# Performance work log

Measured on AMD Instinct MI355X. Metric: run time of the kernel, lower is better.

Reference implementation:

```python
import jax, jax.numpy as jnp
import numpy as np

N_NODES = 262144
N_EDGES = 2097152
N_GRAPHS = 8192
IN_CH = 54
HID = 32
OUT_CH = 64
SLOPE = 0.01  # AttentiveFP uses leaky_relu / GATConv negative_slope=0.01
NUM_TIMESTEPS = 2


def _gru(x, h, wih, whh, bih, bhh):
    # torch.nn.GRUCell semantics
    gi = x @ wih.T + bih
    gh = h @ whh.T + bhh
    ir, iz, inn = jnp.split(gi, 3, axis=-1)
    hr, hz, hn = jnp.split(gh, 3, axis=-1)
    r = jax.nn.sigmoid(ir + hr)
    z = jax.nn.sigmoid(iz + hz)
    n = jnp.tanh(inn + r * hn)
    return (1.0 - z) * n + z * h


def _seg_softmax(a, idx, n):
    # PyG softmax over edges grouped by target index
    m = jax.ops.segment_max(a, idx, num_segments=n)
    e = jnp.exp(a - m[idx])
    s = jax.ops.segment_sum(e, idx, num_segments=n)
    return e / (s[idx] + 1e-16)


def _forward(x, edge_attr,
             lin1_w, lin1_b,
             g_lin1_w, g_lin2_w, g_att_l, g_att_r, g_bias,
             gru1_wih, gru1_whh, gru1_bih, gru1_bhh,
             a_lin_w, a_att_src, a_att_dst, a_bias,
             gru2_wih, gru2_whh, gru2_bih, gru2_bhh,
             m_lin_w, m_att_src, m_att_dst, m_bias,
             gru3_wih, gru3_whh, gru3_bih, gru3_bhh,
             lin2_w, lin2_b,
             edge_index, batch_index):
    src, dst = edge_index[0], edge_index[1]  # j -> i (source_to_target)
    n = x.shape[0]
    # Atom embedding
    x = jax.nn.leaky_relu(x @ lin1_w.T + lin1_b, SLOPE)
    # --- GATEConv (first layer, uses edge features) ---
    xj, xi = x[src], x[dst]
    e = jax.nn.leaky_relu(jnp.concatenate([xj, edge_attr], axis=-1) @ g_lin1_w.T, SLOPE)
    alpha = jax.nn.leaky_relu(e @ g_att_l + xi @ g_att_r, SLOPE)
    alpha = _seg_softmax(alpha, dst, n)
    h = jax.ops.segment_sum((xj @ g_lin2_w.T) * alpha[:, None], dst, num_segments=n) + g_bias
    h = jax.nn.elu(h)
    x = jax.nn.relu(_gru(h, x, gru1_wih, gru1_whh, gru1_bih, gru1_bhh))
    # --- GATConv atom layer (num_layers=2 -> one extra conv) ---
    xt = x @ a_lin_w.T
    al = xt @ a_att_src
    ar = xt @ a_att_dst
    alpha = jax.nn.leaky_relu(al[src] + ar[dst], SLOPE)
    alpha = _seg_softmax(alpha, dst, n)
    h = jax.ops.segment_sum(xt[src] * alpha[:, None], dst, num_segments=n) + a_bias
    h = jax.nn.elu(h)
    x = jax.nn.relu(_gru(h, x, gru2_wih, gru2_whh, gru2_bih, gru2_bhh))
    # --- Molecule readout: iterative GAT attention from nodes to their graph ---
    out = jax.nn.relu(jax.ops.segment_sum(x, batch_index, num_segments=N_GRAPHS))
    xs = x @ m_lin_w.T          # transformed node (source) features, fixed per step
    a_node = xs @ m_att_src     # per-node attention logit contribution
    for _ in range(NUM_TIMESTEPS):
        a_g = (out @ m_lin_w.T) @ m_att_dst  # per-graph contribution
        alpha = jax.nn.leaky_relu(a_node + a_g[batch_index], SLOPE)
        alpha = _seg_softmax(alpha, batch_index, N_GRAPHS)
        h = jax.ops.segment_sum(xs * alpha[:, None], batch_index, num_segments=N_GRAPHS) + m_bias
        h = jax.nn.elu(h)
        out = jax.nn.relu(_gru(h, out, gru3_wih, gru3_whh, gru3_bih, gru3_bhh))
    out = out @ lin2_w.T + lin2_b
    # Mish activation wrapper
    return out * jnp.tanh(jax.nn.softplus(out))


def setup_inputs() -> dict:
    key = jax.random.key(0)
    ks = jax.random.split(key, 24)
    def rn(k, shape, s=0.1):
        return jax.random.normal(k, shape, dtype=jnp.float32) * s
    z = lambda *s: jnp.zeros(s, jnp.float32)
    return {
        "x": jax.random.normal(ks[0], (N_NODES, IN_CH), dtype=jnp.float32),
        "edge_attr": jax.random.normal(ks[1], (N_EDGES, 1), dtype=jnp.float32),
        "edge_index": jax.random.randint(ks[2], (2, N_EDGES), 0, N_NODES, dtype=jnp.int32),
        "batch_index": jnp.sort(jax.random.randint(ks[3], (N_NODES,), 0, N_GRAPHS, dtype=jnp.int32)),
        "lin1_w": rn(ks[4], (HID, IN_CH)), "lin1_b": z(HID),
        "g_lin1_w": rn(ks[5], (HID, HID + 1)),
        "g_lin2_w": rn(ks[6], (HID, HID)),
        "g_att_l": rn(ks[7], (HID,)), "g_att_r": rn(ks[8], (HID,)),
        "g_bias": z(HID),
        "gru1_wih": rn(ks[9], (3 * HID, HID)), "gru1_whh": rn(ks[10], (3 * HID, HID)),
        "gru1_bih": z(3 * HID), "gru1_bhh": z(3 * HID),
        "a_lin_w": rn(ks[11], (HID, HID)),
        "a_att_src": rn(ks[12], (HID,)), "a_att_dst": rn(ks[13], (HID,)),
        "a_bias": z(HID),
        "gru2_wih": rn(ks[14], (3 * HID, HID)), "gru2_whh": rn(ks[15], (3 * HID, HID)),
        "gru2_bih": z(3 * HID), "gru2_bhh": z(3 * HID),
        "m_lin_w": rn(ks[16], (HID, HID)),
        "m_att_src": rn(ks[17], (HID,)), "m_att_dst": rn(ks[18], (HID,)),
        "m_bias": z(HID),
        "gru3_wih": rn(ks[19], (3 * HID, HID)), "gru3_whh": rn(ks[20], (3 * HID, HID)),
        "gru3_bih": z(3 * HID), "gru3_bhh": z(3 * HID),
        "lin2_w": rn(ks[21], (OUT_CH, HID)), "lin2_b": z(OUT_CH),
    }


def reference(x, edge_attr, edge_index, batch_index,
              lin1_w, lin1_b,
              g_lin1_w, g_lin2_w, g_att_l, g_att_r, g_bias,
              gru1_wih, gru1_whh, gru1_bih, gru1_bhh,
              a_lin_w, a_att_src, a_att_dst, a_bias,
              gru2_wih, gru2_whh, gru2_bih, gru2_bhh,
              m_lin_w, m_att_src, m_att_dst, m_bias,
              gru3_wih, gru3_whh, gru3_bih, gru3_bhh,
              lin2_w, lin2_b):
    return _forward(x, edge_attr,
                    lin1_w, lin1_b,
                    g_lin1_w, g_lin2_w, g_att_l, g_att_r, g_bias,
                    gru1_wih, gru1_whh, gru1_bih, gru1_bhh,
                    a_lin_w, a_att_src, a_att_dst, a_bias,
                    gru2_wih, gru2_whh, gru2_bih, gru2_bhh,
                    m_lin_w, m_att_src, m_att_dst, m_bias,
                    gru3_wih, gru3_whh, gru3_bih, gru3_bhh,
                    lin2_w, lin2_b,
                    edge_index, batch_index)
```

## Files before the change

kernel.cpp:

```cpp
#include <hip/hip_runtime.h>
#include <hip/hip_bf16.h>
#include <math.h>

#define NN 262144
#define NE 2097152
#define NG 8192
#define THREADS 256

typedef __hip_bfloat16 bf16;
typedef __attribute__((ext_vector_type(8))) short short8v;
typedef __attribute__((ext_vector_type(4))) float f32x4;

static __device__ __forceinline__ float lrelu(float x){ return x > 0.f ? x : 0.01f*x; }
static __device__ __forceinline__ float eluf(float x){ return x > 0.f ? x : __expf(x) - 1.f; }
static __device__ __forceinline__ float sigm(float x){ return 1.f/(1.f + __expf(-x)); }
static __device__ __forceinline__ float tanh_fast(float x){
  float e = __expf(2.f*x); return 1.f - 2.f/(e + 1.f);
}
static __device__ __forceinline__ float b2f(bf16 v){ return __bfloat162float(v); }
static __device__ __forceinline__ bf16 f2b(float v){ return __float2bfloat16(v); }
static __device__ __forceinline__ float s2f(short s){
  return __uint_as_float(((unsigned int)(unsigned short)s) << 16);
}

static __device__ __forceinline__ unsigned short bfbits(float f){
  union { bf16 b; unsigned short s; } u; u.b = f2b(f); return u.s;
}
static __device__ __forceinline__ unsigned int pack2(float lo, float hi){
  return (unsigned int)bfbits(lo) | ((unsigned int)bfbits(hi) << 16);
}

static __device__ __forceinline__ float redsum32(float t){
  #pragma unroll
  for (int o = 16; o > 0; o >>= 1) t += __shfl_xor(t, o, 32);
  return t;
}

static __device__ __forceinline__ float gru_relu(float hv, float xv, int c,
    const float* __restrict__ wih, const float* __restrict__ whh,
    const float* __restrict__ bih, const float* __restrict__ bhh){
  float gr = bih[c], gz = bih[32+c], gn = bih[64+c];
  float hr = bhh[c], hz = bhh[32+c], hn = bhh[64+c];
  #pragma unroll 8
  for (int k = 0; k < 32; k++){
    float hk = __shfl(hv, k, 32);
    float xk = __shfl(xv, k, 32);
    gr += hk*wih[(     c)*32 + k];
    gz += hk*wih[(32 + c)*32 + k];
    gn += hk*wih[(64 + c)*32 + k];
    hr += xk*whh[(     c)*32 + k];
    hz += xk*whh[(32 + c)*32 + k];
    hn += xk*whh[(64 + c)*32 + k];
  }
  float r = sigm(gr + hr), z = sigm(gz + hz);
  float nn2 = tanh_fast(gn + r*hn);
  return fmaxf((1.f - z)*nn2 + z*xv, 0.f);
}

__global__ __launch_bounds__(THREADS) void k_filli(int* __restrict__ p, int v, int n){
  int i = blockIdx.x*THREADS + threadIdx.x;
  if (i < n) p[i] = v;
}

#define FB_EMBED 512
#define FB_HIST  8192
#define FB_GPTR  1024

__global__ __launch_bounds__(THREADS) void k_front(
    const float* __restrict__ xin, const float* __restrict__ lw, const float* __restrict__ lb,
    const float* __restrict__ w1, const float* __restrict__ w2,
    const float* __restrict__ attr_r, float* __restrict__ X,
    bf16* __restrict__ uv, float* __restrict__ nr,
    const int* __restrict__ ei, int* __restrict__ hist, int* __restrict__ rank,
    const int* __restrict__ batch, int* __restrict__ gptr){
  __shared__ float ol[4][16][33];
  int bid = blockIdx.x;
  if (bid < FB_EMBED){
    int wid  = bid*4 + (threadIdx.x >> 6);
    int wv   = threadIdx.x >> 6;
    int lane = threadIdx.x & 63;
    int cl = lane & 15;
    int kb = lane >> 4;
    short8v BL[2][2], BU[2], BV[2];
    #pragma unroll
    for (int g = 0; g < 2; g++){
      #pragma unroll
      for (int kc = 0; kc < 2; kc++){
        short8v t;
        #pragma unroll
        for (int j = 0; j < 8; j++){
          int k = kc*32 + kb*8 + j;
          t[j] = (k < 54) ? (short)bfbits(lw[(size_t)(g*16+cl)*54 + k]) : (short)0;
        }
        BL[g][kc] = t;
      }
      short8v tu, tv;
      #pragma unroll
      for (int j = 0; j < 8; j++){
        tu[j] = (short)bfbits(w1[(size_t)(g*16+cl)*33 + kb*8 + j]);
        tv[j] = (short)bfbits(w2[(size_t)(g*16+cl)*32 + kb*8 + j]);
      }
      BU[g] = tu; BV[g] = tv;
    }
    float bb0 = lb[cl], bb1 = lb[16+cl];
    float ar0 = attr_r[cl], ar1 = attr_r[16+cl];
    f32x4 zero; zero[0]=0.f; zero[1]=0.f; zero[2]=0.f; zero[3]=0.f;

    for (int t = 0; t < 8; t++){
      int nb = (wid*8 + t)*16;
      const float* xrow = xin + (size_t)(nb + cl)*54;
      short8v Ax0, Ax1;
      const float2* x2 = (const float2*)(xrow + kb*8);
      #pragma unroll
      for (int jj = 0; jj < 4; jj++){
        float2 tvv = x2[jj];
        Ax0[2*jj]   = (short)bfbits(tvv.x);
        Ax0[2*jj+1] = (short)bfbits(tvv.y);
      }
      #pragma unroll
      for (int j = 0; j < 8; j++){
        int k = 32 + kb*8 + j;
        Ax1[j] = (k < 54) ? (short)bfbits(xrow[k]) : (short)0;
      }
      f32x4 a0, a1;
      #pragma unroll
      for (int q = 0; q < 4; q++){ a0[q] = bb0; a1[q] = bb1; }
      f32x4 d0 = __builtin_amdgcn_mfma_f32_16x16x32_bf16(Ax0, BL[0][0], a0, 0, 0, 0);
      d0 = __builtin_amdgcn_mfma_f32_16x16x32_bf16(Ax1, BL[0][1], d0, 0, 0, 0);
      f32x4 d1 = __builtin_amdgcn_mfma_f32_16x16x32_bf16(Ax0, BL[1][0], a1, 0, 0, 0);
      d1 = __builtin_amdgcn_mfma_f32_16x16x32_bf16(Ax1, BL[1][1], d1, 0, 0, 0);
      #pragma unroll
      for (int r = 0; r < 4; r++){ d0[r] = lrelu(d0[r]); d1[r] = lrelu(d1[r]); }
      #pragma unroll
      for (int r = 0; r < 4; r++){
        int node = nb + kb*4 + r;
        float* srow = X + (size_t)node*32;
        srow[cl]      = d0[r];
        srow[16 + cl] = d1[r];
        ol[wv][kb*4 + r][cl]      = d0[r];
        ol[wv][kb*4 + r][16 + cl] = d1[r];
      }
      #pragma unroll
      for (int r = 0; r < 4; r++){
        float vsum = d0[r]*ar0 + d1[r]*ar1;
        vsum += __shfl_xor(vsum, 1, 16);
        vsum += __shfl_xor(vsum, 2, 16);
        vsum += __shfl_xor(vsum, 4, 16);
        vsum += __shfl_xor(vsum, 8, 16);
        if (cl == 0) nr[nb + kb*4 + r] = vsum;
      }
      __syncthreads();
      short8v Ao;
      #pragma unroll
      for (int j = 0; j < 8; j++) Ao[j] = (short)bfbits(ol[wv][cl][kb*8 + j]);
      f32x4 u0 = __builtin_amdgcn_mfma_f32_16x16x32_bf16(Ao, BU[0], zero, 0, 0, 0);
      f32x4 u1 = __builtin_amdgcn_mfma_f32_16x16x32_bf16(Ao, BU[1], zero, 0, 0, 0);
      f32x4 v0 = __builtin_amdgcn_mfma_f32_16x16x32_bf16(Ao, BV[0], zero, 0, 0, 0);
      f32x4 v1 = __builtin_amdgcn_mfma_f32_16x16x32_bf16(Ao, BV[1], zero, 0, 0, 0);
      #pragma unroll
      for (int r = 0; r < 4; r++){
        int node = nb + kb*4 + r;
        bf16* rowp = uv + (size_t)node*64;
        rowp[cl]           = f2b(u0[r]);
        rowp[16 + cl]      = f2b(u1[r]);
        rowp[32 + cl]      = f2b(v0[r]);
        rowp[48 + cl]      = f2b(v1[r]);
      }
      __syncthreads();
    }
  } else if (bid < FB_EMBED + FB_HIST){
    int e = (bid - FB_EMBED)*THREADS + threadIdx.x;
    rank[e] = atomicAdd(hist + ei[NE + e], 1);
  } else {
    int n = (bid - FB_EMBED - FB_HIST)*THREADS + threadIdx.x;
    int bc = batch[n];
    if (n == 0){ for (int g = 0; g <= bc; g++) gptr[g] = 0; }
    else {
      int pb = batch[n-1];
      if (pb != bc) for (int g = pb+1; g <= bc; g++) gptr[g] = n;
    }
    if (n == NN-1){ for (int g = bc+1; g <= NG; g++) gptr[g] = NN; }
  }
}

__global__ __launch_bounds__(THREADS) void k_scan1(const int* __restrict__ hist,
    int* __restrict__ rp1, int* __restrict__ btot){
  __shared__ int sh[THREADS];
  int i = blockIdx.x*THREADS + threadIdx.x;
  int v = hist[i];
  sh[threadIdx.x] = v; __syncthreads();
  #pragma unroll
  for (int off = 1; off < THREADS; off <<= 1){
    int t = (threadIdx.x >= off) ? sh[threadIdx.x - off] : 0;
    __syncthreads(); sh[threadIdx.x] += t; __syncthreads();
  }
  rp1[i] = sh[threadIdx.x] - v;
  if (threadIdx.x == THREADS-1) btot[blockIdx.x] = sh[THREADS-1];
}

__global__ __launch_bounds__(1024) void k_scan2(int* __restrict__ btot){
  __shared__ int sh[1024];
  int i = threadIdx.x;
  int v = btot[i];
  sh[i] = v; __syncthreads();
  for (int off = 1; off < 1024; off <<= 1){
    int t = (i >= off) ? sh[i - off] : 0;
    __syncthreads(); sh[i] += t; __syncthreads();
  }
  btot[i] = sh[i] - v;
}

#define MB_SCAN 1024

__global__ __launch_bounds__(THREADS) void k_mid(const int* __restrict__ rp1,
    const int* __restrict__ btot, int* __restrict__ rowptr,
    const int* __restrict__ ei, const float* __restrict__ ea,
    const int* __restrict__ rank, int2* __restrict__ epk){
  int bid = blockIdx.x;
  if (bid < MB_SCAN){
    int i = bid*THREADS + threadIdx.x;
    rowptr[i] = rp1[i] + btot[i >> 8];
    if (i == 0) rowptr[NN] = NE;
  } else {
    int e = (bid - MB_SCAN)*THREADS + threadIdx.x;
    int d = ei[NE + e];
    int pos = rp1[d] + btot[d >> 8] + rank[e];
    epk[pos] = make_int2(ei[e], __float_as_int(ea[e]));
  }
}

__global__ __launch_bounds__(THREADS) void k_gru_att(const bf16* __restrict__ HV,
    float* __restrict__ S,
    const float* __restrict__ wih, const float* __restrict__ whh,
    const float* __restrict__ bih, const float* __restrict__ bhh,
    const float* __restrict__ attW, const float* __restrict__ att1,
    const float* __restrict__ att2,
    bf16* __restrict__ xt, float* __restrict__ s1, float* __restrict__ s2){
  __shared__ float ol[4][16][33];
  int wid  = (blockIdx.x*THREADS + threadIdx.x) >> 6;
  int wv   = threadIdx.x >> 6;
  int lane = threadIdx.x & 63;
  int cl = lane & 15;
  int kb = lane >> 4;
  short8v BW[12], BT[2];
  #pragma unroll
  for (int g = 0; g < 6; g++){
    const float* wr = wih + (size_t)(g*16 + cl)*32 + kb*8;
    const float* vr = whh + (size_t)(g*16 + cl)*32 + kb*8;
    short8v bw, bv;
    #pragma unroll
    for (int j = 0; j < 8; j++){ bw[j] = (short)bfbits(wr[j]); bv[j] = (short)bfbits(vr[j]); }
    BW[g] = bw; BW[6+g] = bv;
  }
  #pragma unroll
  for (int g = 0; g < 2; g++){
    short8v bt;
    #pragma unroll
    for (int j = 0; j < 8; j++) bt[j] = (short)bfbits(attW[(size_t)(g*16+cl)*32 + kb*8 + j]);
    BT[g] = bt;
  }
  float bI[6], bH[6];
  #pragma unroll
  for (int g = 0; g < 6; g++){ bI[g] = bih[g*16 + cl]; bH[g] = bhh[g*16 + cl]; }
  float a1c0 = att1[cl], a1c1 = att1[16+cl];
  float a2c0 = att2 ? att2[cl] : 0.f, a2c1 = att2 ? att2[16+cl] : 0.f;
  f32x4 zero; zero[0]=0.f; zero[1]=0.f; zero[2]=0.f; zero[3]=0.f;

  for (int t = 0; t < 8; t++){
    int nb = (wid*8 + t) * 16;
    short8v Ah = *(const short8v*)(HV + (size_t)(nb + cl)*32 + kb*8);
    const float* xr = S + (size_t)(nb + cl)*32 + kb*8;
    short8v Ax;
    #pragma unroll
    for (int j = 0; j < 8; j++) Ax[j] = (short)bfbits(xr[j]);
    f32x4 gi[6], gh[6];
    #pragma unroll
    for (int g = 0; g < 6; g++){
      f32x4 a, b;
      #pragma unroll
      for (int q = 0; q < 4; q++){ a[q] = bI[g]; b[q] = bH[g]; }
      gi[g] = __builtin_amdgcn_mfma_f32_16x16x32_bf16(Ah, BW[g],   a, 0, 0, 0);
      gh[g] = __builtin_amdgcn_mfma_f32_16x16x32_bf16(Ax, BW[6+g], b, 0, 0, 0);
    }
    #pragma unroll
    for (int r = 0; r < 4; r++){
      int node = nb + kb*4 + r;
      float* srow = S + (size_t)node*32;
      float x0 = srow[cl], x1 = srow[16 + cl];
      float r0 = sigm(gi[0][r] + gh[0][r]);
      float z0 = sigm(gi[2][r] + gh[2][r]);
      float n0 = tanh_fast(gi[4][r] + r0*gh[4][r]);
      float r1 = sigm(gi[1][r] + gh[1][r]);
      float z1 = sigm(gi[3][r] + gh[3][r]);
      float n1 = tanh_fast(gi[5][r] + r1*gh[5][r]);
      float o0 = fmaxf((1.f - z0)*n0 + z0*x0, 0.f);
      float o1 = fmaxf((1.f - z1)*n1 + z1*x1, 0.f);
      srow[cl]      = o0;
      srow[16 + cl] = o1;
      ol[wv][kb*4 + r][cl]      = o0;
      ol[wv][kb*4 + r][16 + cl] = o1;
    }
    __syncthreads();
    short8v Ao;
    #pragma unroll
    for (int j = 0; j < 8; j++) Ao[j] = (short)bfbits(ol[wv][cl][kb*8 + j]);
    f32x4 t0 = __builtin_amdgcn_mfma_f32_16x16x32_bf16(Ao, BT[0], zero, 0, 0, 0);
    f32x4 t1 = __builtin_amdgcn_mfma_f32_16x16x32_bf16(Ao, BT[1], zero, 0, 0, 0);
    #pragma unroll
    for (int r = 0; r < 4; r++){
      int node = nb + kb*4 + r;
      bf16* xrow = xt + (size_t)node*32;
      xrow[cl]      = f2b(t0[r]);
      xrow[16 + cl] = f2b(t1[r]);
      float p1 = t0[r]*a1c0 + t1[r]*a1c1;
      p1 += __shfl_xor(p1, 1, 16);
      p1 += __shfl_xor(p1, 2, 16);
      p1 += __shfl_xor(p1, 4, 16);
      p1 += __shfl_xor(p1, 8, 16);
      if (cl == 0) s1[node] = p1;
      if (att2){
        float p2 = t0[r]*a2c0 + t1[r]*a2c1;
        p2 += __shfl_xor(p2, 1, 16);
        p2 += __shfl_xor(p2, 2, 16);
        p2 += __shfl_xor(p2, 4, 16);
        p2 += __shfl_xor(p2, 8, 16);
        if (cl == 0) s2[node] = p2;
      }
    }
    __syncthreads();
  }
}

__global__ __launch_bounds__(THREADS) void k_conv(const int* __restrict__ rowptr,
    const int2* __restrict__ epk, const bf16* __restrict__ U,
    const float* __restrict__ w1 , const float* __restrict__ attl,
    const float* __restrict__ alsrc, const float* __restrict__ term,
    const bf16* __restrict__ ROWS, int rstride, int voff,
    const float* __restrict__ bias, bf16* __restrict__ HV){
  int node = blockIdx.x*(THREADS/32) + (threadIdx.x >> 5);
  int c32 = threadIdx.x & 31;
  int ws = rowptr[node], we = rowptr[node+1];
  float tv = term[node];
  float wc[32], at[32];
  if (U){
    #pragma unroll
    for (int j = 0; j < 32; j++){ wc[j] = w1[j*33 + 32]; at[j] = attl[j]; }
  }
  int eg = c32 >> 2, cb = c32 & 3;
  float s = 0.f;
  float acc[8];
  #pragma unroll
  for (int j = 0; j < 8; j++) acc[j] = 0.f;
  for (int p0 = ws; p0 < we; p0 += 32){
    int p = p0 + c32;
    bool ok = p < we;
    int pc = ok ? p : ws;
    int2 pk = epk[pc];
    int siA = pk.x;
    float sc;
    if (U){
      float a = __int_as_float(pk.y);
      const short8v* ur = (const short8v*)(U + (size_t)siA*64);
      sc = 0.f;
      #pragma unroll
      for (int q = 0; q < 4; q++){
        short8v u8 = ur[q];
        #pragma unroll
        for (int j = 0; j < 8; j++)
          sc += at[q*8+j]*lrelu(s2f(u8[j]) + a*wc[q*8+j]);
      }
    } else {
      sc = alsrc[siA];
    }
    float wme = ok ? __expf(lrelu(sc + tv)) : 0.f;
    s += redsum32(wme);
    #pragma unroll
    for (int s8 = 0; s8 < 32; s8 += 8){
      if (p0 + s8 >= we) break;
      float w = __shfl(wme, s8 + eg, 32);
      int si  = __shfl(siA, s8 + eg, 32);
      short8v r8 = *(const short8v*)(ROWS + (size_t)si*rstride + voff + cb*8);
      #pragma unroll
      for (int j = 0; j < 8; j++) acc[j] += s2f(r8[j]) * w;
    }
  }
  float inv = 1.f/(s + 1e-16f);
  #pragma unroll
  for (int j = 0; j < 8; j++){
    acc[j] += __shfl_xor(acc[j], 4, 32);
    acc[j] += __shfl_xor(acc[j], 8, 32);
    acc[j] += __shfl_xor(acc[j], 16, 32);
  }
  if (eg == 0){
    unsigned int o[4];
    #pragma unroll
    for (int j2 = 0; j2 < 4; j2++){
      float h0 = eluf(acc[2*j2  ]*inv + bias[cb*8 + 2*j2  ]);
      float h1 = eluf(acc[2*j2+1]*inv + bias[cb*8 + 2*j2+1]);
      o[j2] = pack2(h0, h1);
    }
    *(uint4*)(HV + (size_t)node*32 + cb*8) = make_uint4(o[0], o[1], o[2], o[3]);
  }
}

__global__ __launch_bounds__(THREADS) void k_readout(const int* __restrict__ gptr,
    const float* __restrict__ X, const float* __restrict__ anode,
    const bf16* __restrict__ XS,
    const float* __restrict__ mw , const float* __restrict__ mattd,
    const float* __restrict__ mbias,
    const float* __restrict__ wih, const float* __restrict__ whh,
    const float* __restrict__ bih, const float* __restrict__ bhh,
    const float* __restrict__ lin2_w, const float* __restrict__ lin2_b,
    float* __restrict__ y){
  int g = blockIdx.x*(THREADS/32) + (threadIdx.x >> 5);
  int c = threadIdx.x & 31;
  int gs = gptr[g], ge = gptr[g+1];
  float out = 0.f;
  for (int n = gs; n < ge; n++) out += X[(size_t)n*32 + c];
  out = fmaxf(out, 0.f);
  float qc = 0.f;
  #pragma unroll
  for (int j = 0; j < 32; j++) qc += mattd[j]*mw[j*32 + c];
  #pragma unroll 1
  for (int t = 0; t < 2; t++){
    float ag = redsum32(out * qc);
    float s = 0.f;
    for (int p0 = gs; p0 < ge; p0 += 32){
      int p = p0 + c;
      float e = (p < ge) ? __expf(lrelu(anode[p] + ag)) : 0.f;
      s += redsum32(e);
    }
    float inv = 1.f/(s + 1e-16f);
    float acc = 0.f;
    int n = gs;
    for (; n + 4 <= ge; n += 4){
      float e0 = __expf(lrelu(anode[n]   + ag));
      float e1 = __expf(lrelu(anode[n+1] + ag));
      float e2 = __expf(lrelu(anode[n+2] + ag));
      float e3 = __expf(lrelu(anode[n+3] + ag));
      acc += b2f(XS[(size_t)(n  )*32 + c])*e0 + b2f(XS[(size_t)(n+1)*32 + c])*e1
           + b2f(XS[(size_t)(n+2)*32 + c])*e2 + b2f(XS[(size_t)(n+3)*32 + c])*e3;
    }
    for (; n < ge; n++)
      acc += b2f(XS[(size_t)n*32 + c]) * __expf(lrelu(anode[n] + ag));
    acc *= inv;
    float hv = eluf(acc + mbias[c]);
    out = gru_relu(hv, out, c, wih, whh, bih, bhh);
  }
  #pragma unroll
  for (int oc2 = 0; oc2 < 2; oc2++){
    int oc = oc2*32 + c;
    float facc = lin2_b[oc];
    const float* wr = lin2_w + (size_t)oc*32;
    #pragma unroll 8
    for (int k = 0; k < 32; k++) facc += __shfl(out, k, 32) * wr[k];
    float sp = fmaxf(facc, 0.f) + log1pf(expf(-fabsf(facc)));
    y[(size_t)g*64 + oc] = facc * tanhf(sp);
  }
}

extern "C" void kernel_launch(void* const* d_in, const int* in_sizes, int n_in,
                              void* d_out, int out_size, void* d_ws, size_t ws_size,
                              hipStream_t stream){
  const float* x_in     = (const float*)d_in[0];
  const float* ea       = (const float*)d_in[1];
  const int*   ei       = (const int*)  d_in[2];
  const int*   batch    = (const int*)  d_in[3];
  const float* lin1_w   = (const float*)d_in[4];
  const float* lin1_b   = (const float*)d_in[5];
  const float* g_lin1_w = (const float*)d_in[6];
  const float* g_lin2_w = (const float*)d_in[7];
  const float* g_att_l  = (const float*)d_in[8];
  const float* g_att_r  = (const float*)d_in[9];
  const float* g_bias   = (const float*)d_in[10];
  const float* gru1_wih = (const float*)d_in[11];
  const float* gru1_whh = (const float*)d_in[12];
  const float* gru1_bih = (const float*)d_in[13];
  const float* gru1_bhh = (const float*)d_in[14];
  const float* a_lin_w  = (const float*)d_in[15];
  const float* a_att_src= (const float*)d_in[16];
  const float* a_att_dst= (const float*)d_in[17];
  const float* a_bias   = (const float*)d_in[18];
  const float* gru2_wih = (const float*)d_in[19];
  const float* gru2_whh = (const float*)d_in[20];
  const float* gru2_bih = (const float*)d_in[21];
  const float* gru2_bhh = (const float*)d_in[22];
  const float* m_lin_w  = (const float*)d_in[23];
  const float* m_att_src= (const float*)d_in[24];
  const float* m_att_dst= (const float*)d_in[25];
  const float* m_bias   = (const float*)d_in[26];
  const float* gru3_wih = (const float*)d_in[27];
  const float* gru3_whh = (const float*)d_in[28];
  const float* gru3_bih = (const float*)d_in[29];
  const float* gru3_bhh = (const float*)d_in[30];
  const float* lin2_w   = (const float*)d_in[31];
  const float* lin2_b   = (const float*)d_in[32];

  float* W = (float*)d_ws;
  float* X     = W;
  bf16*  UV    = (bf16*)(W + 8388608);
  bf16*  XT    = (bf16*)(W + 8388608);
  int2*  EPK   = (int2*) (W + 16777216);
  int*   RP1   = (int*)  (W + 20971520);
  bf16*  BC    = (bf16*) (W + 20971520);
  int*   RANK  = (int*)  (W + 23068672);
  int*   ROWPTR= (int*)  (W + 25165824);
  int*   HIST  = (int*)  (W + 25428032);
  int*   BTOT  = (int*)  (W + 25690176);
  float* NS1   = W + 25691200;
  float* NS2   = W + 25953344;
  int*   GPTR  = (int*)  (W + 26215488);

  dim3 b(THREADS);
  const int gNode  = NN/THREADS;
  const int gNode32= NN/(THREADS/32);
  const int gMFMA  = NN/(16*8*4);
  const int gRO    = NG/(THREADS/32);

  k_filli<<<gNode, b, 0, stream>>>(HIST, 0, NN);

  k_front<<<FB_EMBED + FB_HIST + FB_GPTR, b, 0, stream>>>(
      x_in, lin1_w, lin1_b, g_lin1_w, g_lin2_w, g_att_r, X, UV, NS1,
      ei, HIST, RANK, batch, GPTR);

  k_scan1<<<gNode, b, 0, stream>>>(HIST, RP1, BTOT);
  k_scan2<<<1, 1024, 0, stream>>>(BTOT);
  k_mid<<<MB_SCAN + NE/THREADS, b, 0, stream>>>(RP1, BTOT, ROWPTR, ei, ea, RANK, EPK);

  k_conv<<<gNode32, b, 0, stream>>>(ROWPTR, EPK, UV, g_lin1_w, g_att_l,
      nullptr, NS1, UV, 64, 32, g_bias, BC);
  k_gru_att<<<gMFMA, b, 0, stream>>>(BC, X, gru1_wih, gru1_whh, gru1_bih, gru1_bhh,
      a_lin_w, a_att_src, a_att_dst, XT, NS1, NS2);

  k_conv<<<gNode32, b, 0, stream>>>(ROWPTR, EPK, nullptr, nullptr, nullptr,
      NS1, NS2, XT, 32, 0, a_bias, BC);
  k_gru_att<<<gMFMA, b, 0, stream>>>(BC, X, gru2_wih, gru2_whh, gru2_bih, gru2_bhh,
      m_lin_w, m_att_src, nullptr, XT, NS1, nullptr);

  k_readout<<<gRO, b, 0, stream>>>(GPTR, X, NS1, XT, m_lin_w, m_att_dst, m_bias,
      gru3_wih, gru3_whh, gru3_bih, gru3_bhh, lin2_w, lin2_b, (float*)d_out);
}
```

Baseline: 451.0 us.

## Process four nodes per 32-lane group in conv kernel

The edge-aggregation kernel now assigns 8 lanes per destination node instead of 32, so each 32-lane group handles four nodes at once. With average degree about 8, this is meant to remove idle lanes and the wasted 32-wide edge batches and reductions. The grid shrinks by a factor of four. Per-node loops now take more iterations for high-degree nodes, and nodes within a group can diverge in edge count.

Result: faster. 403.9 us (-10.4%).

```diff
diff --git a/kernel.cpp b/kernel.cpp
--- a/kernel.cpp
+++ b/kernel.cpp
@@ -337,8 +337,11 @@
     const float* __restrict__ alsrc, const float* __restrict__ term,
     const bf16* __restrict__ ROWS, int rstride, int voff,
     const float* __restrict__ bias, bf16* __restrict__ HV){
-  int node = blockIdx.x*(THREADS/32) + (threadIdx.x >> 5);
+  int grp = blockIdx.x*(THREADS/32) + (threadIdx.x >> 5);
   int c32 = threadIdx.x & 31;
+  int sub = c32 >> 3;
+  int l8  = c32 & 7;
+  int node = grp*4 + sub;
   int ws = rowptr[node], we = rowptr[node+1];
   float tv = term[node];
   float wc[32], at[32];
@@ -346,13 +349,13 @@
     #pragma unroll
     for (int j = 0; j < 32; j++){ wc[j] = w1[j*33 + 32]; at[j] = attl[j]; }
   }
-  int eg = c32 >> 2, cb = c32 & 3;
-  float s = 0.f;
+  int eh = l8 >> 2, cb = l8 & 3;
+  float sl = 0.f;
   float acc[8];
   #pragma unroll
   for (int j = 0; j < 8; j++) acc[j] = 0.f;
-  for (int p0 = ws; p0 < we; p0 += 32){
-    int p = p0 + c32;
+  for (int p0 = ws; p0 < we; p0 += 8){
+    int p = p0 + l8;
     bool ok = p < we;
     int pc = ok ? p : ws;
     int2 pk = epk[pc];
@@ -373,25 +376,25 @@
       sc = alsrc[siA];
     }
     float wme = ok ? __expf(lrelu(sc + tv)) : 0.f;
-    s += redsum32(wme);
-    #pragma unroll
-    for (int s8 = 0; s8 < 32; s8 += 8){
-      if (p0 + s8 >= we) break;
-      float w = __shfl(wme, s8 + eg, 32);
-      int si  = __shfl(siA, s8 + eg, 32);
+    sl += wme;
+    #pragma unroll
+    for (int se = 0; se < 4; se++){
+      if (p0 + se*2 >= we) break;
+      int lsrc = sub*8 + se*2 + eh;
+      float w = __shfl(wme, lsrc, 32);
+      int si  = __shfl(siA, lsrc, 32);
       short8v r8 = *(const short8v*)(ROWS + (size_t)si*rstride + voff + cb*8);
       #pragma unroll
       for (int j = 0; j < 8; j++) acc[j] += s2f(r8[j]) * w;
     }
   }
-  float inv = 1.f/(s + 1e-16f);
-  #pragma unroll
-  for (int j = 0; j < 8; j++){
-    acc[j] += __shfl_xor(acc[j], 4, 32);
-    acc[j] += __shfl_xor(acc[j], 8, 32);
-    acc[j] += __shfl_xor(acc[j], 16, 32);
-  }
-  if (eg == 0){
+  sl += __shfl_xor(sl, 1, 32);
+  sl += __shfl_xor(sl, 2, 32);
+  sl += __shfl_xor(sl, 4, 32);
+  float inv = 1.f/(sl + 1e-16f);
+  #pragma unroll
+  for (int j = 0; j < 8; j++) acc[j] += __shfl_xor(acc[j], 4, 32);
+  if (eh == 0){
     unsigned int o[4];
     #pragma unroll
     for (int j2 = 0; j2 < 4; j2++){
@@ -513,7 +516,7 @@
 
   dim3 b(THREADS);
   const int gNode  = NN/THREADS;
-  const int gNode32= NN/(THREADS/32);
+  const int gConv  = NN/32;
   const int gMFMA  = NN/(16*8*4);
   const int gRO    = NG/(THREADS/32);
 
@@ -527,12 +530,12 @@
   k_scan2<<<1, 1024, 0, stream>>>(BTOT);
   k_mid<<<MB_SCAN + NE/THREADS, b, 0, stream>>>(RP1, BTOT, ROWPTR, ei, ea, RANK, EPK);
 
-  k_conv<<<gNode32, b, 0, stream>>>(ROWPTR, EPK, UV, g_lin1_w, g_att_l,
+  k_conv<<<gConv, b, 0, stream>>>(ROWPTR, EPK, UV, g_lin1_w, g_att_l,
       nullptr, NS1, UV, 64, 32, g_bias, BC);
   k_gru_att<<<gMFMA, b, 0, stream>>>(BC, X, gru1_wih, gru1_whh, gru1_bih, gru1_bhh,
       a_lin_w, a_att_src, a_att_dst, XT, NS1, NS2);
 
-  k_conv<<<gNode32, b, 0, stream>>>(ROWPTR, EPK, nullptr, nullptr, nullptr,
+  k_conv<<<gConv, b, 0, stream>>>(ROWPTR, EPK, nullptr, nullptr, nullptr,
       NS1, NS2, XT, 32, 0, a_bias, BC);
   k_gru_att<<<gMFMA, b, 0, stream>>>(BC, X, gru2_wih, gru2_whh, gru2_bih, gru2_bhh,
       m_lin_w, m_att_src, nullptr, XT, NS1, nullptr);
```
